# Kernel tuning notes

Hardware: AMD Instinct MI355X
Metric: run time of the kernel (lower is better)

## Reference

```python
import jax, jax.numpy as jnp
import numpy as np

B, S, T, N, D, L = 8192, 10, 3, 65536, 128, 2  # batch, neigh len, node types, table size, embed_d, layers
NEG_SLOPE = 0.01  # torch LeakyReLU default


def setup_inputs() -> dict:
    key = jax.random.key(0)
    ks = jax.random.split(key, 6)
    return {
        "emb": jax.random.normal(ks[0], (T, N, D), jnp.float32) * 0.02,
        "Wih": jax.random.normal(ks[1], (L, T, D, D), jnp.float32) / np.sqrt(D).astype(np.float32),
        "Whh": jax.random.normal(ks[2], (L, T, D, D), jnp.float32) / np.sqrt(D).astype(np.float32),
        "bih": jnp.full((L, T, D), 0.1, jnp.float32),
        "bhh": jnp.full((L, T, D), 0.1, jnp.float32),
        "w_att": jax.random.normal(ks[3], (L, 2 * D), jnp.float32) / np.sqrt(2 * D).astype(np.float32),
        "ids": jax.random.randint(ks[4], (B,), 0, N),
        "neigh_idx": jax.random.randint(ks[5], (T, B, S), 0, N),
    }


def _rnn_mean(x, Wih_l, Whh_l, bih_l, bhh_l):
    """x: [T,B,S,D] neighbor embeds. torch nn.RNN(tanh): h_s = tanh(x_s@Wih^T + bih + h@Whh^T + bhh).
    Returns mean of all hidden states over time: [T,B,D]."""
    xs = jnp.moveaxis(x, 2, 0)  # [S, T, B, D]
    h0 = jnp.zeros((T, B, D), x.dtype)

    def step(h, x_s):
        h = jnp.tanh(jnp.einsum('tbd,ted->tbe', x_s, Wih_l) + bih_l[:, None, :]
                     + jnp.einsum('tbd,ted->tbe', h, Whh_l) + bhh_l[:, None, :])
        return h, h

    _, hs = jax.lax.scan(step, h0, xs)  # [S, T, B, D]
    return hs.mean(axis=0)


def reference(emb, Wih, Whh, bih, bhh, w_att, ids, neigh_idx):
    cur = emb[0][ids]  # [B, D] target node type = 0
    # per-type neighbor gather from base embedding tables (same each layer, as in source)
    neigh = jax.vmap(lambda e, i: e[i])(emb, neigh_idx)  # [T, B, S, D]
    for l in range(L):
        agg = _rnn_mean(neigh, Wih[l], Whh[l], bih[l], bhh[l])  # [T, B, D]
        cands = jnp.moveaxis(jnp.concatenate([cur[None], agg], axis=0), 0, 1)  # [B, 1+T, D]
        feat = jnp.concatenate(
            [jnp.broadcast_to(cur[:, None, :], cands.shape), cands], axis=-1)  # [B, 1+T, 2D]
        scores = feat @ w_att[l]  # [B, 1+T]
        w = jax.nn.softmax(scores, axis=1)[..., None]
        cur = jax.nn.leaky_relu(jnp.sum(w * cands, axis=1), NEG_SLOPE)
    return cur
```

## Files before the change

### kernel.cpp

```cpp
#include <hip/hip_runtime.h>
#include <hip/hip_bf16.h>

#define NB   8192
#define NS   10
#define NT   3
#define NN   65536
#define ND   128
#define NL   2

typedef __attribute__((ext_vector_type(8))) short bf16x8;
typedef __attribute__((ext_vector_type(4))) float f32x4;

__device__ __forceinline__ unsigned int f2bf(float f) {
    unsigned int x = __float_as_uint(f);
    return (x + 0x7FFFu + ((x >> 16) & 1u)) >> 16;
}
__device__ __forceinline__ unsigned int pk2(float lo, float hi) {
    unsigned int r;
    asm("v_cvt_pk_bf16_f32 %0, %1, %2" : "=v"(r) : "v"(lo), "v"(hi));
    return r;
}
__device__ __forceinline__ float fast_tanh(float x) {
    float e = __expf(2.0f * x);
    return 1.0f - __fdividef(2.0f, e + 1.0f);
}

__global__ __launch_bounds__(256, 2)
void rnn_kernel(const float* __restrict__ emb, const float* __restrict__ Wih,
                const float* __restrict__ Whh, const float* __restrict__ bih,
                const float* __restrict__ bhh, const int* __restrict__ nidx,
                float* __restrict__ agg)
{
    __shared__ __align__(16) unsigned short Xs[64 * 128];
    __shared__ __align__(16) unsigned short Hs[64 * 128];
    char* xb = (char*)Xs;
    char* hb = (char*)Hs;

    const int bid = blockIdx.x;
    const int l   = bid / (NT * 128);
    const int t   = (bid / 128) % NT;
    const int b0  = (bid % 128) * 64;

    const int tid  = threadIdx.x;
    const int w    = tid >> 6;
    const int lane = tid & 63;
    const int l16  = lane & 15;
    const int lg   = lane >> 4;
    const int e0   = w * 32;
    const int rx   = l16 & 7;

    const float* Wih_lt = Wih + (size_t)(l * NT + t) * ND * ND;
    const float* Whh_lt = Whh + (size_t)(l * NT + t) * ND * ND;
    const float* bih_lt = bih + (size_t)(l * NT + t) * ND;
    const float* bhh_lt = bhh + (size_t)(l * NT + t) * ND;

    const int srow = tid >> 2;
    const int sq   = tid & 3;
    const int ssw  = srow & 7;

    const int* ip = nidx + ((size_t)t * NB + b0 + srow) * NS;

    float4 P[8];
    {
        int idx0 = ip[0];
        const float* src = emb + ((size_t)t * NN + idx0) * ND + sq * 32;
        #pragma unroll
        for (int c = 0; c < 4; ++c) {
            P[2 * c]     = *(const float4*)(src + c * 8);
            P[2 * c + 1] = *(const float4*)(src + c * 8 + 4);
        }
    }

    bf16x8 Af[2][8];
    #pragma unroll
    for (int mt = 0; mt < 2; ++mt) {
        #pragma unroll
        for (int kc = 0; kc < 8; ++kc) {
            const float* Wsrc = (kc < 4) ? Wih_lt : Whh_lt;
            const float* srcp = Wsrc + (size_t)(e0 + mt * 16 + l16) * ND + (kc & 3) * 32 + lg * 8;
            float4 p0 = *(const float4*)(srcp);
            float4 p1 = *(const float4*)(srcp + 4);
            bf16x8 v;
            v[0] = (short)f2bf(p0.x); v[1] = (short)f2bf(p0.y);
            v[2] = (short)f2bf(p0.z); v[3] = (short)f2bf(p0.w);
            v[4] = (short)f2bf(p1.x); v[5] = (short)f2bf(p1.y);
            v[6] = (short)f2bf(p1.z); v[7] = (short)f2bf(p1.w);
            Af[mt][kc] = v;
        }
    }

    float bias[2][4];
    #pragma unroll
    for (int mt = 0; mt < 2; ++mt)
        #pragma unroll
        for (int i = 0; i < 4; ++i) {
            int e = e0 + mt * 16 + lg * 4 + i;
            bias[mt][i] = bih_lt[e] + bhh_lt[e];
        }

    f32x4 zero4; zero4[0] = 0.f; zero4[1] = 0.f; zero4[2] = 0.f; zero4[3] = 0.f;
    f32x4 Ag[4][2];
    #pragma unroll
    for (int nt = 0; nt < 4; ++nt) { Ag[nt][0] = zero4; Ag[nt][1] = zero4; }

    for (int s = 0; s < NS; ++s) {
        #pragma unroll
        for (int c = 0; c < 4; ++c) {
            int4 pk;
            pk.x = (int)pk2(P[2 * c].x,     P[2 * c].y);
            pk.y = (int)pk2(P[2 * c].z,     P[2 * c].w);
            pk.z = (int)pk2(P[2 * c + 1].x, P[2 * c + 1].y);
            pk.w = (int)pk2(P[2 * c + 1].z, P[2 * c + 1].w);
            int chunk = (sq * 4 + c) ^ ssw;
            *(int4*)(xb + srow * 256 + (chunk << 4)) = pk;
        }
        if (s + 1 < NS) {
            int idxn = ip[s + 1];
            const float* src = emb + ((size_t)t * NN + idxn) * ND + sq * 32;
            #pragma unroll
            for (int c = 0; c < 4; ++c) {
                P[2 * c]     = *(const float4*)(src + c * 8);
                P[2 * c + 1] = *(const float4*)(src + c * 8 + 4);
            }
        }
        __syncthreads();

        f32x4 acc[4][2];
        #pragma unroll
        for (int nt = 0; nt < 4; ++nt) { acc[nt][0] = zero4; acc[nt][1] = zero4; }

        #pragma unroll
        for (int nt = 0; nt < 4; ++nt) {
            const int r = nt * 16 + l16;
            #pragma unroll
            for (int kc = 0; kc < 8; ++kc) {
                if (kc < 4 || s > 0) {
                    const char* buf = (kc < 4) ? xb : hb;
                    int chunk = ((kc & 3) * 4 + lg) ^ rx;
                    bf16x8 bf = *(const bf16x8*)(buf + r * 256 + (chunk << 4));
                    acc[nt][0] = __builtin_amdgcn_mfma_f32_16x16x32_bf16(Af[0][kc], bf, acc[nt][0], 0, 0, 0);
                    acc[nt][1] = __builtin_amdgcn_mfma_f32_16x16x32_bf16(Af[1][kc], bf, acc[nt][1], 0, 0, 0);
                }
            }
        }
        __syncthreads();

        #pragma unroll
        for (int nt = 0; nt < 4; ++nt) {
            const int r = nt * 16 + l16;
            #pragma unroll
            for (int mt = 0; mt < 2; ++mt) {
                f32x4 h;
                #pragma unroll
                for (int i = 0; i < 4; ++i)
                    h[i] = fast_tanh(acc[nt][mt][i] + bias[mt][i]);
                Ag[nt][mt] += h;
                int2 pk;
                pk.x = (int)pk2(h[0], h[1]);
                pk.y = (int)pk2(h[2], h[3]);
                int estart = e0 + mt * 16 + lg * 4;
                int chunk  = (estart >> 3) ^ rx;
                *(int2*)(hb + r * 256 + (chunk << 4) + (estart & 7) * 2) = pk;
            }
        }
    }

    float* aggp = agg + ((size_t)(l * NT + t) * NB + b0) * ND;
    #pragma unroll
    for (int nt = 0; nt < 4; ++nt) {
        int b = nt * 16 + l16;
        #pragma unroll
        for (int mt = 0; mt < 2; ++mt) {
            f32x4 v = Ag[nt][mt] * 0.1f;
            *(f32x4*)(aggp + (size_t)b * ND + e0 + mt * 16 + lg * 4) = v;
        }
    }
}

__global__ __launch_bounds__(256)
void att_kernel(const float* __restrict__ emb, const int* __restrict__ ids,
                const float* __restrict__ w_att, const float* __restrict__ agg,
                float* __restrict__ cur, const int l)
{
    const int wid  = threadIdx.x >> 6;
    const int lane = threadIdx.x & 63;
    const int b    = blockIdx.x * 4 + wid;

    const float* waH  = w_att + l * 2 * ND;
    const float* waT  = waH + ND;
    const float* crow = (l == 0) ? (emb + (size_t)ids[b] * ND) : (cur + (size_t)b * ND);
    const float* ab   = agg + ((size_t)(l * NT) * NB + b) * ND;

    const float c1 = crow[lane], c2 = crow[lane + 64];
    const float h1 = waH[lane],  h2 = waH[lane + 64];
    const float t1 = waT[lane],  t2 = waT[lane + 64];
    float g1[3], g2[3];
    #pragma unroll
    for (int tt = 0; tt < 3; ++tt) {
        g1[tt] = ab[(size_t)tt * NB * ND + lane];
        g2[tt] = ab[(size_t)tt * NB * ND + lane + 64];
    }

    float dH = c1 * h1 + c2 * h2;
    float dc = c1 * t1 + c2 * t2;
    float d0 = g1[0] * t1 + g2[0] * t2;
    float d1 = g1[1] * t1 + g2[1] * t2;
    float d2 = g1[2] * t1 + g2[2] * t2;
    #pragma unroll
    for (int off = 32; off > 0; off >>= 1) {
        dH += __shfl_xor(dH, off);
        dc += __shfl_xor(dc, off);
        d0 += __shfl_xor(d0, off);
        d1 += __shfl_xor(d1, off);
        d2 += __shfl_xor(d2, off);
    }

    float s0 = dH + dc, s1 = dH + d0, s2 = dH + d1, s3 = dH + d2;
    float m  = fmaxf(fmaxf(s0, s1), fmaxf(s2, s3));
    float q0 = __expf(s0 - m), q1 = __expf(s1 - m), q2 = __expf(s2 - m), q3 = __expf(s3 - m);
    float inv = __fdividef(1.0f, q0 + q1 + q2 + q3);
    float w0 = q0 * inv, w1 = q1 * inv, w2 = q2 * inv, w3 = q3 * inv;

    float o1 = w0 * c1 + w1 * g1[0] + w2 * g1[1] + w3 * g1[2];
    float o2 = w0 * c2 + w1 * g2[0] + w2 * g2[1] + w3 * g2[2];
    o1 = (o1 > 0.f) ? o1 : 0.01f * o1;
    o2 = (o2 > 0.f) ? o2 : 0.01f * o2;

    float* orow = cur + (size_t)b * ND;
    orow[lane]      = o1;
    orow[lane + 64] = o2;
}

extern "C" void kernel_launch(void* const* d_in, const int* in_sizes, int n_in,
                              void* d_out, int out_size, void* d_ws, size_t ws_size,
                              hipStream_t stream)
{
    const float* emb  = (const float*)d_in[0];
    const float* Wih  = (const float*)d_in[1];
    const float* Whh  = (const float*)d_in[2];
    const float* bih  = (const float*)d_in[3];
    const float* bhh  = (const float*)d_in[4];
    const float* watt = (const float*)d_in[5];
    const int*   ids  = (const int*)d_in[6];
    const int*   nidx = (const int*)d_in[7];

    float* cur = (float*)d_out;
    float* agg = (float*)d_ws;

    rnn_kernel<<<dim3(NL * NT * 128), dim3(256), 0, stream>>>(emb, Wih, Whh, bih, bhh, nidx, agg);
    att_kernel<<<dim3(NB / 4), dim3(256), 0, stream>>>(emb, ids, watt, agg, cur, 0);
    att_kernel<<<dim3(NB / 4), dim3(256), 0, stream>>>(emb, ids, watt, agg, cur, 1);
}
```

Baseline: 93.27 us.

## Shrink RNN tiles to 32 rows, raise occupancy, preload indices, lighter barriers

Each RNN block now handles 32 batch rows instead of 64. That halves shared memory and accumulator registers, so launch bounds can request 4 blocks per CU and there are twice as many blocks. The gather is split so each thread loads 16 floats per row, all 10 neighbor indices are preloaded into registers, and the weight conversion uses the hardware packed bf16 convert. __syncthreads is replaced by an lgkmcnt wait plus s_barrier, which avoids waiting on the in-flight global prefetch. The trade-off is that each block reuses its register-resident weights across fewer rows, so weight loading and conversion are repeated more often overall.

```diff
diff --git a/kernel.cpp b/kernel.cpp
--- a/kernel.cpp
+++ b/kernel.cpp
@@ -7,14 +7,11 @@
 #define NN   65536
 #define ND   128
 #define NL   2
+#define ROWS 32
 
 typedef __attribute__((ext_vector_type(8))) short bf16x8;
 typedef __attribute__((ext_vector_type(4))) float f32x4;
 
-__device__ __forceinline__ unsigned int f2bf(float f) {
-    unsigned int x = __float_as_uint(f);
-    return (x + 0x7FFFu + ((x >> 16) & 1u)) >> 16;
-}
 __device__ __forceinline__ unsigned int pk2(float lo, float hi) {
     unsigned int r;
     asm("v_cvt_pk_bf16_f32 %0, %1, %2" : "=v"(r) : "v"(lo), "v"(hi));
@@ -24,22 +21,25 @@
     float e = __expf(2.0f * x);
     return 1.0f - __fdividef(2.0f, e + 1.0f);
 }
-
-__global__ __launch_bounds__(256, 2)
+__device__ __forceinline__ void bar_lgkm() {
+    asm volatile("s_waitcnt lgkmcnt(0)\n\ts_barrier" ::: "memory");
+}
+
+__global__ __launch_bounds__(256, 4)
 void rnn_kernel(const float* __restrict__ emb, const float* __restrict__ Wih,
                 const float* __restrict__ Whh, const float* __restrict__ bih,
                 const float* __restrict__ bhh, const int* __restrict__ nidx,
                 float* __restrict__ agg)
 {
-    __shared__ __align__(16) unsigned short Xs[64 * 128];
-    __shared__ __align__(16) unsigned short Hs[64 * 128];
+    __shared__ __align__(16) unsigned short Xs[ROWS * 128];
+    __shared__ __align__(16) unsigned short Hs[ROWS * 128];
     char* xb = (char*)Xs;
     char* hb = (char*)Hs;
 
     const int bid = blockIdx.x;
-    const int l   = bid / (NT * 128);
-    const int t   = (bid / 128) % NT;
-    const int b0  = (bid % 128) * 64;
+    const int l   = bid / (NT * (NB / ROWS));
+    const int t   = (bid / (NB / ROWS)) % NT;
+    const int b0  = (bid % (NB / ROWS)) * ROWS;
 
     const int tid  = threadIdx.x;
     const int w    = tid >> 6;
@@ -54,21 +54,20 @@
     const float* bih_lt = bih + (size_t)(l * NT + t) * ND;
     const float* bhh_lt = bhh + (size_t)(l * NT + t) * ND;
 
-    const int srow = tid >> 2;
-    const int sq   = tid & 3;
+    const int srow = tid >> 3;
+    const int sq   = tid & 7;
     const int ssw  = srow & 7;
 
     const int* ip = nidx + ((size_t)t * NB + b0 + srow) * NS;
-
-    float4 P[8];
+    int idxs[NS];
+    #pragma unroll
+    for (int s = 0; s < NS; ++s) idxs[s] = ip[s];
+
+    float4 P[4];
     {
-        int idx0 = ip[0];
-        const float* src = emb + ((size_t)t * NN + idx0) * ND + sq * 32;
-        #pragma unroll
-        for (int c = 0; c < 4; ++c) {
-            P[2 * c]     = *(const float4*)(src + c * 8);
-            P[2 * c + 1] = *(const float4*)(src + c * 8 + 4);
-        }
+        const float* src = emb + ((size_t)t * NN + idxs[0]) * ND + sq * 16;
+        #pragma unroll
+        for (int c = 0; c < 4; ++c) P[c] = *(const float4*)(src + c * 4);
     }
 
     bf16x8 Af[2][8];
@@ -80,12 +79,12 @@
             const float* srcp = Wsrc + (size_t)(e0 + mt * 16 + l16) * ND + (kc & 3) * 32 + lg * 8;
             float4 p0 = *(const float4*)(srcp);
             float4 p1 = *(const float4*)(srcp + 4);
-            bf16x8 v;
-            v[0] = (short)f2bf(p0.x); v[1] = (short)f2bf(p0.y);
-            v[2] = (short)f2bf(p0.z); v[3] = (short)f2bf(p0.w);
-            v[4] = (short)f2bf(p1.x); v[5] = (short)f2bf(p1.y);
-            v[6] = (short)f2bf(p1.z); v[7] = (short)f2bf(p1.w);
-            Af[mt][kc] = v;
+            int4 a;
+            a.x = (int)pk2(p0.x, p0.y);
+            a.y = (int)pk2(p0.z, p0.w);
+            a.z = (int)pk2(p1.x, p1.y);
+            a.w = (int)pk2(p1.z, p1.w);
+            Af[mt][kc] = *(bf16x8*)&a;
         }
     }
 
@@ -99,38 +98,34 @@
         }
 
     f32x4 zero4; zero4[0] = 0.f; zero4[1] = 0.f; zero4[2] = 0.f; zero4[3] = 0.f;
-    f32x4 Ag[4][2];
-    #pragma unroll
-    for (int nt = 0; nt < 4; ++nt) { Ag[nt][0] = zero4; Ag[nt][1] = zero4; }
+    f32x4 Ag[2][2];
+    #pragma unroll
+    for (int nt = 0; nt < 2; ++nt) { Ag[nt][0] = zero4; Ag[nt][1] = zero4; }
 
     for (int s = 0; s < NS; ++s) {
         #pragma unroll
-        for (int c = 0; c < 4; ++c) {
+        for (int j = 0; j < 2; ++j) {
             int4 pk;
-            pk.x = (int)pk2(P[2 * c].x,     P[2 * c].y);
-            pk.y = (int)pk2(P[2 * c].z,     P[2 * c].w);
-            pk.z = (int)pk2(P[2 * c + 1].x, P[2 * c + 1].y);
-            pk.w = (int)pk2(P[2 * c + 1].z, P[2 * c + 1].w);
-            int chunk = (sq * 4 + c) ^ ssw;
+            pk.x = (int)pk2(P[2 * j].x,     P[2 * j].y);
+            pk.y = (int)pk2(P[2 * j].z,     P[2 * j].w);
+            pk.z = (int)pk2(P[2 * j + 1].x, P[2 * j + 1].y);
+            pk.w = (int)pk2(P[2 * j + 1].z, P[2 * j + 1].w);
+            int chunk = (2 * sq + j) ^ ssw;
             *(int4*)(xb + srow * 256 + (chunk << 4)) = pk;
         }
         if (s + 1 < NS) {
-            int idxn = ip[s + 1];
-            const float* src = emb + ((size_t)t * NN + idxn) * ND + sq * 32;
+            const float* src = emb + ((size_t)t * NN + idxs[s + 1]) * ND + sq * 16;
             #pragma unroll
-            for (int c = 0; c < 4; ++c) {
-                P[2 * c]     = *(const float4*)(src + c * 8);
-                P[2 * c + 1] = *(const float4*)(src + c * 8 + 4);
-            }
-        }
-        __syncthreads();
-
-        f32x4 acc[4][2];
-        #pragma unroll
-        for (int nt = 0; nt < 4; ++nt) { acc[nt][0] = zero4; acc[nt][1] = zero4; }
-
-        #pragma unroll
-        for (int nt = 0; nt < 4; ++nt) {
+            for (int c = 0; c < 4; ++c) P[c] = *(const float4*)(src + c * 4);
+        }
+        bar_lgkm();
+
+        f32x4 acc[2][2];
+        #pragma unroll
+        for (int nt = 0; nt < 2; ++nt) { acc[nt][0] = zero4; acc[nt][1] = zero4; }
+
+        #pragma unroll
+        for (int nt = 0; nt < 2; ++nt) {
             const int r = nt * 16 + l16;
             #pragma unroll
             for (int kc = 0; kc < 8; ++kc) {
@@ -143,11 +138,12 @@
                 }
             }
         }
-        __syncthreads();
-
-        #pragma unroll
-        for (int nt = 0; nt < 4; ++nt) {
+        bar_lgkm();
+
+        #pragma unroll
+        for (int nt = 0; nt < 2; ++nt) {
             const int r = nt * 16 + l16;
+            const int rr = r & 7;
             #pragma unroll
             for (int mt = 0; mt < 2; ++mt) {
                 f32x4 h;
@@ -159,7 +155,7 @@
                 pk.x = (int)pk2(h[0], h[1]);
                 pk.y = (int)pk2(h[2], h[3]);
                 int estart = e0 + mt * 16 + lg * 4;
-                int chunk  = (estart >> 3) ^ rx;
+                int chunk  = (estart >> 3) ^ rr;
                 *(int2*)(hb + r * 256 + (chunk << 4) + (estart & 7) * 2) = pk;
             }
         }
@@ -167,7 +163,7 @@
 
     float* aggp = agg + ((size_t)(l * NT + t) * NB + b0) * ND;
     #pragma unroll
-    for (int nt = 0; nt < 4; ++nt) {
+    for (int nt = 0; nt < 2; ++nt) {
         int b = nt * 16 + l16;
         #pragma unroll
         for (int mt = 0; mt < 2; ++mt) {
@@ -247,7 +243,7 @@
     float* cur = (float*)d_out;
     float* agg = (float*)d_ws;
 
-    rnn_kernel<<<dim3(NL * NT * 128), dim3(256), 0, stream>>>(emb, Wih, Whh, bih, bhh, nidx, agg);
+    rnn_kernel<<<dim3(NL * NT * (NB / ROWS)), dim3(256), 0, stream>>>(emb, Wih, Whh, bih, bhh, nidx, agg);
     att_kernel<<<dim3(NB / 4), dim3(256), 0, stream>>>(emb, ids, watt, agg, cur, 0);
     att_kernel<<<dim3(NB / 4), dim3(256), 0, stream>>>(emb, ids, watt, agg, cur, 1);
 }
```

After: 187.6 us. 101% more time.
